# Kernel optimization log

Hardware: AMD Instinct MI355X
Metric: run time of the kernel (lower is better)

Reference implementation:

```python
import math
import jax, jax.numpy as jnp
import numpy as np

NUM_HEADS = 16
EPS = 1e-6


def _rotate_half(t):
    t1, t2 = jnp.split(t, 2, axis=-1)
    return jnp.concatenate([-t2, t1], axis=-1)


def _rmsnorm(t, w):
    # compute in fp32 like the torch module, then cast back and apply affine
    x32 = t.astype(jnp.float32)
    r = jax.lax.rsqrt(jnp.mean(x32 * x32, axis=-1, keepdims=True) + EPS)
    return (x32 * r).astype(t.dtype) * w


def setup_inputs() -> dict:
    key = jax.random.key(0)
    ks = jax.random.split(key, 12)
    B, N, C, T = 8, 1024, 1024, 1024
    hd2 = (C // NUM_HEADS) // 2  # 32
    inp = {
        "x": jax.random.normal(ks[0], (B, N, C), jnp.float32),
        "temb": jax.random.normal(ks[1], (B, T), jnp.float32),
        "cos_y": jax.random.uniform(ks[2], (1, 1, N, hd2), jnp.float32, -1.0, 1.0),
        "sin_y": jax.random.uniform(ks[3], (1, 1, N, hd2), jnp.float32, -1.0, 1.0),
        "cos_x": jax.random.uniform(ks[4], (1, 1, N, hd2), jnp.float32, -1.0, 1.0),
        "sin_x": jax.random.uniform(ks[5], (1, 1, N, hd2), jnp.float32, -1.0, 1.0),
        # params; weights stored (in, out) so y = x @ W + b (== torch x @ W.T)
        "Wqkv": jax.random.normal(ks[6], (C, 3 * C), jnp.float32) * 0.02,
        "bqkv": jnp.zeros((3 * C,), jnp.float32),
        "Wt": jax.random.normal(ks[7], (T, 3 * C), jnp.float32) * 0.02,
        "bt": jnp.zeros((3 * C,), jnp.float32),
        "Wp": jax.random.normal(ks[8], (C, C), jnp.float32) * 0.02,
        "bp": jnp.zeros((C,), jnp.float32),
        "qn_w": jnp.ones((C // NUM_HEADS,), jnp.float32),
        "kn_w": jnp.ones((C // NUM_HEADS,), jnp.float32),
    }
    return inp


def reference(x, temb, cos_y, sin_y, cos_x, sin_x,
              Wqkv, bqkv, Wt, bt, Wp, bp, qn_w, kn_w):
    B, N, C = x.shape
    H = NUM_HEADS
    hd = C // H
    # fused QKV projection + additive time conditioning
    qkv = x @ Wqkv + bqkv + (temb @ Wt + bt)[:, None, :]         # [B,N,3C]
    qkv = qkv.reshape(B, N, 3, H, hd).transpose(2, 0, 3, 1, 4)    # [3,B,H,N,hd]
    q, k, v = qkv[0], qkv[1], qkv[2]
    # per-head QK RMSNorm with affine
    q = _rmsnorm(q, qn_w)
    k = _rmsnorm(k, kn_w)
    # axial 2D RoPE on the y-half and x-half of head_dim
    qy, qx = jnp.split(q, 2, axis=-1)
    ky, kx = jnp.split(k, 2, axis=-1)
    qy = qy * cos_y + _rotate_half(qy) * sin_y
    ky = ky * cos_y + _rotate_half(ky) * sin_y
    qx = qx * cos_x + _rotate_half(qx) * sin_x
    kx = kx * cos_x + _rotate_half(kx) * sin_x
    q = jnp.concatenate([qy, qx], axis=-1)
    k = jnp.concatenate([ky, kx], axis=-1)
    # scaled dot-product attention (no dropout at eval)
    scale = 1.0 / math.sqrt(hd)
    scores = jnp.einsum('bhqd,bhkd->bhqk', q, k) * scale
    attn = jax.nn.softmax(scores, axis=-1)
    out = jnp.einsum('bhqk,bhkd->bhqd', attn, v)                  # [B,H,N,hd]
    out = out.transpose(0, 2, 1, 3).reshape(B, N, C)
    return out @ Wp + bp
```

## Files before the change

kernel.cpp:

```cpp
#include <hip/hip_runtime.h>
#include <cstdint>

typedef unsigned short u16;
typedef __bf16 bf16x8 __attribute__((ext_vector_type(8)));
typedef float f32x4 __attribute__((ext_vector_type(4)));

__device__ __forceinline__ u16 f2bf(float f) {
  __bf16 h = (__bf16)f;
  return __builtin_bit_cast(u16, h);
}
__device__ __forceinline__ float bf2f(u16 u) {
  union { uint32_t u; float f; } v; v.u = ((uint32_t)u) << 16;
  return v.f;
}

__device__ __forceinline__ void gload16(const void* g, const void* l) {
  __builtin_amdgcn_global_load_lds(
      (const __attribute__((address_space(1))) uint32_t*)(uintptr_t)g,
      (__attribute__((address_space(3))) uint32_t*)(uintptr_t)l, 16, 0, 0);
}

__device__ __forceinline__ f32x4 mfma16(bf16x8 a, bf16x8 b, f32x4 c) {
  return __builtin_amdgcn_mfma_f32_16x16x32_bf16(a, b, c, 0, 0, 0);
}

__device__ __forceinline__ int swz(int row, int col) {
  return row * 64 + ((((col >> 3) ^ (row & 7)) << 3) | (col & 7));
}

__global__ __launch_bounds__(256)
void k_cvt(const float* __restrict__ src, u16* __restrict__ dst, int n4) {
  int i = blockIdx.x * 256 + threadIdx.x;
  if (i >= n4) return;
  float4 v = ((const float4*)src)[i];
  union { u16 s[4]; uint2 u; } o;
  o.s[0] = f2bf(v.x); o.s[1] = f2bf(v.y); o.s[2] = f2bf(v.z); o.s[3] = f2bf(v.w);
  ((uint2*)dst)[i] = o.u;
}

__global__ __launch_bounds__(256)
void k_transpose(const float* __restrict__ src, u16* __restrict__ dst, int R, int Cc) {
  __shared__ u16 t[64 * 66];
  int r0 = blockIdx.y * 64, c0 = blockIdx.x * 64;
  #pragma unroll
  for (int i = 0; i < 16; i++) {
    int e = i * 256 + threadIdx.x;
    int rl = e >> 6, cl = e & 63;
    t[cl * 66 + rl] = f2bf(src[(size_t)(r0 + rl) * Cc + c0 + cl]);
  }
  __syncthreads();
  #pragma unroll
  for (int i = 0; i < 16; i++) {
    int e = i * 256 + threadIdx.x;
    int ro = e >> 6, co = e & 63;
    dst[(size_t)(c0 + ro) * R + r0 + co] = t[ro * 66 + co];
  }
}

__global__ __launch_bounds__(256)
void k_temb_part(const float* __restrict__ temb, const float* __restrict__ Wt,
                 float* __restrict__ part) {
  const int j = blockIdx.x * 256 + threadIdx.x;
  const int k0 = blockIdx.y * 32;
  float acc[8];
  #pragma unroll
  for (int b = 0; b < 8; b++) acc[b] = 0.f;
  #pragma unroll 4
  for (int k = k0; k < k0 + 32; k++) {
    float wv = Wt[(size_t)k * 3072 + j];
    #pragma unroll
    for (int b = 0; b < 8; b++) acc[b] += temb[b * 1024 + k] * wv;
  }
  float* p = part + (size_t)blockIdx.y * 24576 + j;
  #pragma unroll
  for (int b = 0; b < 8; b++) p[b * 3072] = acc[b];
}

__global__ __launch_bounds__(256)
void k_temb_red(const float* __restrict__ part, const float* __restrict__ bt,
                const float* __restrict__ bqkv, float* __restrict__ tcomb) {
  const int j = blockIdx.x * 256 + threadIdx.x;
  const int b = blockIdx.y;
  const float* p = part + b * 3072 + j;
  float a = bt[j] + bqkv[j];
  #pragma unroll
  for (int kt = 0; kt < 32; kt++) a += p[(size_t)kt * 24576];
  tcomb[b * 3072 + j] = a;
}

template <int MODE>
__global__ __launch_bounds__(512, 2)
void k_gemm(const u16* __restrict__ A, const u16* __restrict__ Bt,
            u16* __restrict__ outb, float* __restrict__ outf,
            const float* __restrict__ bias, int K, int Ntot) {
  __shared__ __align__(16) u16 As[3][128 * 64];
  __shared__ __align__(16) u16 Bs[3][256 * 64];

  const int nb = (int)gridDim.x;
  const int bid = (int)blockIdx.x;
  const int sb = (bid & 7) * (nb >> 3) + (bid >> 3);
  const int NBN = Ntot >> 8;
  const int m0 = (sb / NBN) * 128;
  const int n0 = (sb % NBN) * 256;

  const int lane = threadIdx.x & 63;
  const int w = threadIdx.x >> 6;
  const int wm = w >> 2;
  const int wn = w & 3;
  const int l15 = lane & 15;
  const int g8 = (lane >> 4) * 8;
  const int lr = lane >> 3;
  const int schunk = ((lane & 7) ^ lr) * 8;

  const u16* Ag = A + (size_t)(m0 + w * 16 + lr) * K + schunk;
  const u16* Bg = Bt + (size_t)(n0 + lr) * K + schunk;

  f32x4 acc[4][4];
  #pragma unroll
  for (int i = 0; i < 4; i++)
    #pragma unroll
    for (int j = 0; j < 4; j++) acc[i][j] = (f32x4){0.f, 0.f, 0.f, 0.f};

  auto stageA_Blo = [&](int kt_, int buf_) {
    const int ko = kt_ << 6;
    #pragma unroll
    for (int t = 0; t < 2; t++) {
      int r0 = w * 16 + t * 8;
      gload16(Ag + (size_t)(t * 8) * K + ko, &As[buf_][r0 * 64]);
    }
    #pragma unroll
    for (int t = 0; t < 2; t++) {
      int f0 = w * 16 + t * 8;
      int r0 = (f0 >> 5) * 64 + (f0 & 31);
      gload16(Bg + (size_t)r0 * K + ko, &Bs[buf_][r0 * 64]);
    }
  };
  auto stageBhi = [&](int kt_, int buf_) {
    const int ko = kt_ << 6;
    #pragma unroll
    for (int t = 0; t < 2; t++) {
      int f0 = w * 16 + t * 8;
      int r0 = (f0 >> 5) * 64 + 32 + (f0 & 31);
      gload16(Bg + (size_t)r0 * K + ko, &Bs[buf_][r0 * 64]);
    }
  };

  const int NT = K >> 6;
  stageA_Blo(0, 0); stageBhi(0, 0);
  stageA_Blo(1, 1); stageBhi(1, 1);
  asm volatile("s_waitcnt vmcnt(8)" ::: "memory");
  __builtin_amdgcn_s_barrier();
  asm volatile("" ::: "memory");

  int cur = 0;
  for (int kt = 0; kt < NT; kt++) {
    const int nxtbuf = cur + 2 >= 3 ? cur - 1 : cur + 2;

    bf16x8 af[2][4], bfr[2][4];
    #pragma unroll
    for (int s = 0; s < 2; s++)
      #pragma unroll
      for (int mf = 0; mf < 4; mf++)
        af[s][mf] = *(const bf16x8*)&As[cur][swz(wm * 64 + mf * 16 + l15, s * 32 + g8)];
    #pragma unroll
    for (int s = 0; s < 2; s++)
      #pragma unroll
      for (int nf = 0; nf < 2; nf++)
        bfr[s][nf] = *(const bf16x8*)&Bs[cur][swz(wn * 64 + nf * 16 + l15, s * 32 + g8)];
    if (kt + 2 < NT) stageA_Blo(kt + 2, nxtbuf);
    if (kt <= NT - 2) asm volatile("s_waitcnt vmcnt(6)" ::: "memory");
    else              asm volatile("s_waitcnt vmcnt(0)" ::: "memory");
    __builtin_amdgcn_s_barrier();
    asm volatile("" ::: "memory");
    __builtin_amdgcn_s_setprio(1);
    #pragma unroll
    for (int s = 0; s < 2; s++)
      #pragma unroll
      for (int mf = 0; mf < 4; mf++)
        #pragma unroll
        for (int nf = 0; nf < 2; nf++)
          acc[mf][nf] = mfma16(af[s][mf], bfr[s][nf], acc[mf][nf]);
    __builtin_amdgcn_s_setprio(0);

    #pragma unroll
    for (int s = 0; s < 2; s++)
      #pragma unroll
      for (int nf = 2; nf < 4; nf++)
        bfr[s][nf] = *(const bf16x8*)&Bs[cur][swz(wn * 64 + nf * 16 + l15, s * 32 + g8)];
    if (kt + 2 < NT) stageBhi(kt + 2, nxtbuf);
    if (kt < NT - 2)       asm volatile("s_waitcnt vmcnt(6)" ::: "memory");
    else if (kt == NT - 2) asm volatile("s_waitcnt vmcnt(2)" ::: "memory");
    else                   asm volatile("s_waitcnt vmcnt(0)" ::: "memory");
    __builtin_amdgcn_s_barrier();
    asm volatile("" ::: "memory");
    __builtin_amdgcn_s_setprio(1);
    #pragma unroll
    for (int s = 0; s < 2; s++)
      #pragma unroll
      for (int mf = 0; mf < 4; mf++)
        #pragma unroll
        for (int nf = 2; nf < 4; nf++)
          acc[mf][nf] = mfma16(af[s][mf], bfr[s][nf], acc[mf][nf]);
    __builtin_amdgcn_s_setprio(0);

    cur = cur + 1 >= 3 ? 0 : cur + 1;
  }

  const int rl = (lane >> 4) * 4;
  #pragma unroll
  for (int mf = 0; mf < 4; mf++) {
    #pragma unroll
    for (int nf = 0; nf < 4; nf++) {
      #pragma unroll
      for (int r = 0; r < 4; r++) {
        int grow = m0 + wm * 64 + mf * 16 + rl + r;
        int gcol = n0 + wn * 64 + nf * 16 + l15;
        float v = acc[mf][nf][r];
        if (MODE == 0) {
          int b = grow >> 10;
          v += bias[b * Ntot + gcol];
          outb[(size_t)grow * Ntot + gcol] = f2bf(v);
        } else {
          v += bias[gcol];
          outf[(size_t)grow * Ntot + gcol] = v;
        }
      }
    }
  }
}

__global__ __launch_bounds__(256)
void k_rrv(const u16* __restrict__ qkv,
           const float* __restrict__ cos_y, const float* __restrict__ sin_y,
           const float* __restrict__ cos_x, const float* __restrict__ sin_x,
           const float* __restrict__ qn_w, const float* __restrict__ kn_w,
           u16* __restrict__ Qo, u16* __restrict__ Ko, u16* __restrict__ VT) {
  __shared__ u16 t[64 * 68];
  const int n0 = blockIdx.x * 64, h = blockIdx.y, b = blockIdx.z;
  const int bh = b * 16 + h;
  const int lane = threadIdx.x & 63, w = threadIdx.x >> 6;
  const int l15 = lane & 15, lg = lane >> 4;
  float4 qw = *(const float4*)(qn_w + l15 * 4);
  float4 kw = *(const float4*)(kn_w + l15 * 4);
  const float sgn = (lane & 4) ? 1.0f : -1.0f;
  const float* ct = (lane & 8) ? cos_x : cos_y;
  const float* st = (lane & 8) ? sin_x : sin_y;
  const float QSCALE = 0.18033688011112042f;

  #pragma unroll
  for (int rr = 0; rr < 4; rr++) {
    int row = n0 + w * 16 + rr * 4 + lg;
    size_t src = (size_t)(b * 1024 + row) * 3072 + h * 64 + l15 * 4;
    uint2 qu = *(const uint2*)(qkv + src);
    uint2 ku = *(const uint2*)(qkv + src + 1024);
    float q[4], k[4];
    q[0] = bf2f((u16)qu.x); q[1] = bf2f((u16)(qu.x >> 16));
    q[2] = bf2f((u16)qu.y); q[3] = bf2f((u16)(qu.y >> 16));
    k[0] = bf2f((u16)ku.x); k[1] = bf2f((u16)(ku.x >> 16));
    k[2] = bf2f((u16)ku.y); k[3] = bf2f((u16)(ku.y >> 16));
    float sq = q[0]*q[0] + q[1]*q[1] + q[2]*q[2] + q[3]*q[3];
    float sk = k[0]*k[0] + k[1]*k[1] + k[2]*k[2] + k[3]*k[3];
    #pragma unroll
    for (int m = 1; m < 16; m <<= 1) {
      sq += __shfl_xor(sq, m);
      sk += __shfl_xor(sk, m);
    }
    float rq = rsqrtf(sq * (1.0f / 64.0f) + 1e-6f);
    float rk = rsqrtf(sk * (1.0f / 64.0f) + 1e-6f);
    float4 cc = *(const float4*)(ct + (size_t)row * 32 + (lane & 7) * 4);
    float4 ss = *(const float4*)(st + (size_t)row * 32 + (lane & 7) * 4);
    float qn[4], kn[4];
    qn[0] = q[0]*rq*qw.x; qn[1] = q[1]*rq*qw.y; qn[2] = q[2]*rq*qw.z; qn[3] = q[3]*rq*qw.w;
    kn[0] = k[0]*rk*kw.x; kn[1] = k[1]*rk*kw.y; kn[2] = k[2]*rk*kw.z; kn[3] = k[3]*rk*kw.w;
    float c[4] = {cc.x, cc.y, cc.z, cc.w};
    float s[4] = {ss.x, ss.y, ss.z, ss.w};
    union { u16 e[4]; uint2 u; } oq, ok;
    #pragma unroll
    for (int j = 0; j < 4; j++) {
      float qp = __shfl_xor(qn[j], 4);
      float kp = __shfl_xor(kn[j], 4);
      oq.e[j] = f2bf((qn[j] * c[j] + sgn * qp * s[j]) * QSCALE);
      ok.e[j] = f2bf(kn[j] * c[j] + sgn * kp * s[j]);
    }
    size_t dst = ((size_t)bh * 1024 + row) * 64 + l15 * 4;
    *(uint2*)(Qo + dst) = oq.u;
    *(uint2*)(Ko + dst) = ok.u;
  }

  #pragma unroll
  for (int i = 0; i < 4; i++) {
    int e = i * 256 + threadIdx.x;
    int n = e >> 4, dc = e & 15;
    uint2 v = *(const uint2*)(qkv + (size_t)(b * 1024 + n0 + n) * 3072 + 2048 + h * 64 + dc * 4);
    t[(dc * 4 + 0) * 68 + n] = (u16)v.x;
    t[(dc * 4 + 1) * 68 + n] = (u16)(v.x >> 16);
    t[(dc * 4 + 2) * 68 + n] = (u16)v.y;
    t[(dc * 4 + 3) * 68 + n] = (u16)(v.y >> 16);
  }
  __syncthreads();
  #pragma unroll
  for (int i = 0; i < 4; i++) {
    int e = i * 256 + threadIdx.x;
    int d = e >> 4, nc = e & 15;
    const u16* p = &t[d * 68 + nc * 4];
    uint2 o;
    o.x = (uint32_t)p[0] | ((uint32_t)p[1] << 16);
    o.y = (uint32_t)p[2] | ((uint32_t)p[3] << 16);
    *(uint2*)(VT + ((size_t)bh * 64 + d) * 1024 + n0 + nc * 4) = o;
  }
}

__global__ __launch_bounds__(256, 2)
void k_attn(const u16* __restrict__ Q, const u16* __restrict__ Kb,
            const u16* __restrict__ VT, u16* __restrict__ Ob) {
  __shared__ u16 Ks[2][4096], VTs[2][4096], Ps[4][2048];
  const int lane = threadIdx.x & 63;
  const int w = threadIdx.x >> 6;
  const int bh = blockIdx.x;
  const int qt = blockIdx.y;
  const int b = bh >> 4, h = bh & 15;
  const size_t base = (size_t)bh * 65536;
  const int q0 = qt * 128;
  const int scol = ((lane & 7) ^ (lane >> 3)) * 8;
  const int lr = lane >> 3;

  bf16x8 aq[2][2];
  #pragma unroll
  for (int i = 0; i < 2; i++)
    #pragma unroll
    for (int s = 0; s < 2; s++)
      aq[i][s] = *(const bf16x8*)(Q + base +
          (size_t)(q0 + w * 32 + i * 16 + (lane & 15)) * 64 + s * 32 + (lane >> 4) * 8);

  f32x4 acc_o[2][4];
  float lpar[2][4];
  #pragma unroll
  for (int i = 0; i < 2; i++)
    #pragma unroll
    for (int r = 0; r < 4; r++) {
      acc_o[i][r] = (f32x4){0.f, 0.f, 0.f, 0.f};
      lpar[i][r] = 0.f;
    }

  #pragma unroll
  for (int tt = 0; tt < 2; tt++) {
    int t = w * 2 + tt;
    gload16(Kb + base + (size_t)(8 * t + lr) * 64 + scol, &Ks[0][t * 512]);
    gload16(VT + base + (size_t)(8 * t + lr) * 1024 + scol, &VTs[0][t * 512]);
  }

  for (int it = 0; it < 16; it++) {
    __syncthreads();
    const int cur = it & 1;
    if (it < 15) {
      const int nxt = cur ^ 1;
      const int j1 = (it + 1) * 64;
      #pragma unroll
      for (int tt = 0; tt < 2; tt++) {
        int t = w * 2 + tt;
        gload16(Kb + base + (size_t)(j1 + 8 * t + lr) * 64 + scol, &Ks[nxt][t * 512]);
        gload16(VT + base + (size_t)(8 * t + lr) * 1024 + j1 + scol, &VTs[nxt][t * 512]);
      }
    }
    const u16* K_ = Ks[cur];
    const u16* V_ = VTs[cur];

    f32x4 accs[2][4];
    #pragma unroll
    for (int i = 0; i < 2; i++)
      #pragma unroll
      for (int nt = 0; nt < 4; nt++) accs[i][nt] = (f32x4){0.f, 0.f, 0.f, 0.f};
    #pragma unroll
    for (int s = 0; s < 2; s++) {
      bf16x8 bk[4];
      #pragma unroll
      for (int nt = 0; nt < 4; nt++)
        bk[nt] = *(const bf16x8*)&K_[swz(nt * 16 + (lane & 15), s * 32 + (lane >> 4) * 8)];
      #pragma unroll
      for (int i = 0; i < 2; i++)
        #pragma unroll
        for (int nt = 0; nt < 4; nt++)
          accs[i][nt] = mfma16(aq[i][s], bk[nt], accs[i][nt]);
    }

    #pragma unroll
    for (int i = 0; i < 2; i++) {
      #pragma unroll
      for (int nt = 0; nt < 4; nt++) {
        #pragma unroll
        for (int r = 0; r < 4; r++) {
          float p = __builtin_amdgcn_exp2f(accs[i][nt][r]);
          lpar[i][r] += p;
          Ps[w][swz(i * 16 + (lane >> 4) * 4 + r, nt * 16 + (lane & 15))] = f2bf(p);
        }
      }
    }
    asm volatile("s_waitcnt lgkmcnt(0)" ::: "memory");

    #pragma unroll
    for (int s = 0; s < 2; s++) {
      bf16x8 bv[4];
      #pragma unroll
      for (int dt = 0; dt < 4; dt++)
        bv[dt] = *(const bf16x8*)&V_[swz(dt * 16 + (lane & 15), s * 32 + (lane >> 4) * 8)];
      #pragma unroll
      for (int i = 0; i < 2; i++) {
        bf16x8 ap = *(const bf16x8*)&Ps[w][swz(i * 16 + (lane & 15), s * 32 + (lane >> 4) * 8)];
        #pragma unroll
        for (int dt = 0; dt < 4; dt++)
          acc_o[i][dt] = mfma16(ap, bv[dt], acc_o[i][dt]);
      }
    }
  }

  #pragma unroll
  for (int i = 0; i < 2; i++) {
    float inv[4];
    #pragma unroll
    for (int r = 0; r < 4; r++) {
      float l = lpar[i][r];
      #pragma unroll
      for (int m = 1; m < 16; m <<= 1) l += __shfl_xor(l, m);
      inv[r] = 1.0f / l;
    }
    #pragma unroll
    for (int dt = 0; dt < 4; dt++)
      #pragma unroll
      for (int r = 0; r < 4; r++) {
        int row = q0 + w * 32 + i * 16 + (lane >> 4) * 4 + r;
        int col = h * 64 + dt * 16 + (lane & 15);
        Ob[((size_t)b * 1024 + row) * 1024 + col] = f2bf(acc_o[i][dt][r] * inv[r]);
      }
  }
}

extern "C" void kernel_launch(void* const* d_in, const int* in_sizes, int n_in,
                              void* d_out, int out_size, void* d_ws, size_t ws_size,
                              hipStream_t stream) {
  const float* x     = (const float*)d_in[0];
  const float* temb  = (const float*)d_in[1];
  const float* cos_y = (const float*)d_in[2];
  const float* sin_y = (const float*)d_in[3];
  const float* cos_x = (const float*)d_in[4];
  const float* sin_x = (const float*)d_in[5];
  const float* Wqkv  = (const float*)d_in[6];
  const float* bqkv  = (const float*)d_in[7];
  const float* Wt    = (const float*)d_in[8];
  const float* bt    = (const float*)d_in[9];
  const float* Wp    = (const float*)d_in[10];
  const float* bp    = (const float*)d_in[11];
  const float* qn_w  = (const float*)d_in[12];
  const float* kn_w  = (const float*)d_in[13];
  float* out = (float*)d_out;

  char* ws = (char*)d_ws;
  u16*   x_bf  = (u16*)(ws);
  u16*   WqkvT = (u16*)(ws + 16777216);
  u16*   WpT   = (u16*)(ws + 23068672);
  float* tcomb = (float*)(ws + 25165824);
  u16*   qkv   = (u16*)(ws + 25264128);
  u16*   Qb    = (u16*)(ws + 75595776);
  u16*   Kb    = (u16*)(ws + 92372992);
  u16*   VTb   = (u16*)(ws + 109150208);
  float* tpart = (float*)(ws + 125927424);
  u16*   att   = x_bf;

  k_cvt<<<8192, 256, 0, stream>>>(x, x_bf, 8192 * 1024 / 4);
  k_transpose<<<dim3(48, 16), 256, 0, stream>>>(Wqkv, WqkvT, 1024, 3072);
  k_transpose<<<dim3(16, 16), 256, 0, stream>>>(Wp, WpT, 1024, 1024);
  k_temb_part<<<dim3(12, 32), 256, 0, stream>>>(temb, Wt, tpart);
  k_temb_red<<<dim3(12, 8), 256, 0, stream>>>(tpart, bt, bqkv, tcomb);
  k_gemm<0><<<dim3(768), 512, 0, stream>>>(x_bf, WqkvT, qkv, nullptr, tcomb, 1024, 3072);
  k_rrv<<<dim3(16, 16, 8), 256, 0, stream>>>(qkv, cos_y, sin_y, cos_x, sin_x,
                                             qn_w, kn_w, Qb, Kb, VTb);
  k_attn<<<dim3(128, 8), 256, 0, stream>>>(Qb, Kb, VTb, att);
  k_gemm<1><<<dim3(256), 512, 0, stream>>>(att, WpT, nullptr, out, bp, 1024, 1024);
}
```

Baseline: 284.0 us.

## Merge prep kernels into one launch, fold temb reduction into GEMM, prioritize attention MFMAs

```diff
diff --git a/kernel.cpp b/kernel.cpp
--- a/kernel.cpp
+++ b/kernel.cpp
@@ -28,20 +28,9 @@
   return row * 64 + ((((col >> 3) ^ (row & 7)) << 3) | (col & 7));
 }
 
-__global__ __launch_bounds__(256)
-void k_cvt(const float* __restrict__ src, u16* __restrict__ dst, int n4) {
-  int i = blockIdx.x * 256 + threadIdx.x;
-  if (i >= n4) return;
-  float4 v = ((const float4*)src)[i];
-  union { u16 s[4]; uint2 u; } o;
-  o.s[0] = f2bf(v.x); o.s[1] = f2bf(v.y); o.s[2] = f2bf(v.z); o.s[3] = f2bf(v.w);
-  ((uint2*)dst)[i] = o.u;
-}
-
-__global__ __launch_bounds__(256)
-void k_transpose(const float* __restrict__ src, u16* __restrict__ dst, int R, int Cc) {
-  __shared__ u16 t[64 * 66];
-  int r0 = blockIdx.y * 64, c0 = blockIdx.x * 64;
+__device__ __forceinline__ void transpose64(const float* __restrict__ src,
+                                            u16* __restrict__ dst, int R, int Cc,
+                                            int r0, int c0, u16* t) {
   #pragma unroll
   for (int i = 0; i < 16; i++) {
     int e = i * 256 + threadIdx.x;
@@ -58,43 +47,60 @@
 }
 
 __global__ __launch_bounds__(256)
-void k_temb_part(const float* __restrict__ temb, const float* __restrict__ Wt,
-                 float* __restrict__ part) {
-  const int j = blockIdx.x * 256 + threadIdx.x;
-  const int k0 = blockIdx.y * 32;
-  float acc[8];
-  #pragma unroll
-  for (int b = 0; b < 8; b++) acc[b] = 0.f;
-  #pragma unroll 4
-  for (int k = k0; k < k0 + 32; k++) {
-    float wv = Wt[(size_t)k * 3072 + j];
-    #pragma unroll
-    for (int b = 0; b < 8; b++) acc[b] += temb[b * 1024 + k] * wv;
-  }
-  float* p = part + (size_t)blockIdx.y * 24576 + j;
-  #pragma unroll
-  for (int b = 0; b < 8; b++) p[b * 3072] = acc[b];
-}
-
-__global__ __launch_bounds__(256)
-void k_temb_red(const float* __restrict__ part, const float* __restrict__ bt,
-                const float* __restrict__ bqkv, float* __restrict__ tcomb) {
-  const int j = blockIdx.x * 256 + threadIdx.x;
-  const int b = blockIdx.y;
-  const float* p = part + b * 3072 + j;
-  float a = bt[j] + bqkv[j];
-  #pragma unroll
-  for (int kt = 0; kt < 32; kt++) a += p[(size_t)kt * 24576];
-  tcomb[b * 3072 + j] = a;
+void k_prep(const float* __restrict__ x, u16* __restrict__ x_bf,
+            const float* __restrict__ Wqkv, u16* __restrict__ WqkvT,
+            const float* __restrict__ Wp, u16* __restrict__ WpT,
+            const float* __restrict__ temb, const float* __restrict__ Wt,
+            float* __restrict__ tpart) {
+  __shared__ u16 t[64 * 66];
+  int bid = blockIdx.x;
+  if (bid < 8192) {
+    int i = bid * 256 + threadIdx.x;
+    float4 v = ((const float4*)x)[i];
+    union { u16 s[4]; uint2 u; } o;
+    o.s[0] = f2bf(v.x); o.s[1] = f2bf(v.y); o.s[2] = f2bf(v.z); o.s[3] = f2bf(v.w);
+    ((uint2*)x_bf)[i] = o.u;
+    return;
+  }
+  bid -= 8192;
+  if (bid < 768) {
+    transpose64(Wqkv, WqkvT, 1024, 3072, (bid / 48) * 64, (bid % 48) * 64, t);
+    return;
+  }
+  bid -= 768;
+  if (bid < 256) {
+    transpose64(Wp, WpT, 1024, 1024, (bid / 16) * 64, (bid % 16) * 64, t);
+    return;
+  }
+  bid -= 256;
+  {
+    const int j = (bid % 12) * 256 + threadIdx.x;
+    const int k0 = (bid / 12) * 32;
+    float acc[8];
+    #pragma unroll
+    for (int b = 0; b < 8; b++) acc[b] = 0.f;
+    #pragma unroll 4
+    for (int k = k0; k < k0 + 32; k++) {
+      float wv = Wt[(size_t)k * 3072 + j];
+      #pragma unroll
+      for (int b = 0; b < 8; b++) acc[b] += temb[b * 1024 + k] * wv;
+    }
+    float* p = tpart + (size_t)(bid / 12) * 24576 + j;
+    #pragma unroll
+    for (int b = 0; b < 8; b++) p[b * 3072] = acc[b];
+  }
 }
 
 template <int MODE>
 __global__ __launch_bounds__(512, 2)
 void k_gemm(const u16* __restrict__ A, const u16* __restrict__ Bt,
             u16* __restrict__ outb, float* __restrict__ outf,
-            const float* __restrict__ bias, int K, int Ntot) {
+            const float* __restrict__ bias,
+            const float* __restrict__ bt, const float* __restrict__ bqkv,
+            const float* __restrict__ tpart, int K, int Ntot) {
   __shared__ __align__(16) u16 As[3][128 * 64];
   __shared__ __align__(16) u16 Bs[3][256 * 64];
+  __shared__ float tcs[256];
 
   const int nb = (int)gridDim.x;
   const int bid = (int)blockIdx.x;
@@ -114,6 +120,18 @@
 
   const u16* Ag = A + (size_t)(m0 + w * 16 + lr) * K + schunk;
   const u16* Bg = Bt + (size_t)(n0 + lr) * K + schunk;
+
+  if (MODE == 0) {
+    if (threadIdx.x < 256) {
+      const int bidx = m0 >> 10;
+      const int j = n0 + (int)threadIdx.x;
+      float a = bt[j] + bqkv[j];
+      #pragma unroll
+      for (int kt = 0; kt < 32; kt++) a += tpart[(size_t)kt * 24576 + bidx * 3072 + j];
+      tcs[threadIdx.x] = a;
+    }
+    asm volatile("" ::: "memory");
+  }
 
   f32x4 acc[4][4];
   #pragma unroll
@@ -217,8 +235,7 @@
         int gcol = n0 + wn * 64 + nf * 16 + l15;
         float v = acc[mf][nf][r];
         if (MODE == 0) {
-          int b = grow >> 10;
-          v += bias[b * Ntot + gcol];
+          v += tcs[wn * 64 + nf * 16 + l15];
           outb[(size_t)grow * Ntot + gcol] = f2bf(v);
         } else {
           v += bias[gcol];
@@ -376,11 +393,13 @@
       #pragma unroll
       for (int nt = 0; nt < 4; nt++)
         bk[nt] = *(const bf16x8*)&K_[swz(nt * 16 + (lane & 15), s * 32 + (lane >> 4) * 8)];
+      __builtin_amdgcn_s_setprio(1);
       #pragma unroll
       for (int i = 0; i < 2; i++)
         #pragma unroll
         for (int nt = 0; nt < 4; nt++)
           accs[i][nt] = mfma16(aq[i][s], bk[nt], accs[i][nt]);
+      __builtin_amdgcn_s_setprio(0);
     }
 
     #pragma unroll
@@ -403,13 +422,15 @@
       #pragma unroll
       for (int dt = 0; dt < 4; dt++)
         bv[dt] = *(const bf16x8*)&V_[swz(dt * 16 + (lane & 15), s * 32 + (lane >> 4) * 8)];
-      #pragma unroll
-      for (int i = 0; i < 2; i++) {
-        bf16x8 ap = *(const bf16x8*)&Ps[w][swz(i * 16 + (lane & 15), s * 32 + (lane >> 4) * 8)];
-        #pragma unroll
-        for (int dt = 0; dt < 4; dt++)
-          acc_o[i][dt] = mfma16(ap, bv[dt], acc_o[i][dt]);
+      bf16x8 ap0 = *(const bf16x8*)&Ps[w][swz(0 * 16 + (lane & 15), s * 32 + (lane >> 4) * 8)];
+      bf16x8 ap1 = *(const bf16x8*)&Ps[w][swz(1 * 16 + (lane & 15), s * 32 + (lane >> 4) * 8)];
+      __builtin_amdgcn_s_setprio(1);
+      #pragma unroll
+      for (int dt = 0; dt < 4; dt++) {
+        acc_o[0][dt] = mfma16(ap0, bv[dt], acc_o[0][dt]);
+        acc_o[1][dt] = mfma16(ap1, bv[dt], acc_o[1][dt]);
       }
+      __builtin_amdgcn_s_setprio(0);
     }
   }
 
@@ -457,7 +478,6 @@
   u16*   x_bf  = (u16*)(ws);
   u16*   WqkvT = (u16*)(ws + 16777216);
   u16*   WpT   = (u16*)(ws + 23068672);
-  float* tcomb = (float*)(ws + 25165824);
   u16*   qkv   = (u16*)(ws + 25264128);
   u16*   Qb    = (u16*)(ws + 75595776);
   u16*   Kb    = (u16*)(ws + 92372992);
@@ -465,14 +485,12 @@
   float* tpart = (float*)(ws + 125927424);
   u16*   att   = x_bf;
 
-  k_cvt<<<8192, 256, 0, stream>>>(x, x_bf, 8192 * 1024 / 4);
-  k_transpose<<<dim3(48, 16), 256, 0, stream>>>(Wqkv, WqkvT, 1024, 3072);
-  k_transpose<<<dim3(16, 16), 256, 0, stream>>>(Wp, WpT, 1024, 1024);
-  k_temb_part<<<dim3(12, 32), 256, 0, stream>>>(temb, Wt, tpart);
-  k_temb_red<<<dim3(12, 8), 256, 0, stream>>>(tpart, bt, bqkv, tcomb);
-  k_gemm<0><<<dim3(768), 512, 0, stream>>>(x_bf, WqkvT, qkv, nullptr, tcomb, 1024, 3072);
+  k_prep<<<9600, 256, 0, stream>>>(x, x_bf, Wqkv, WqkvT, Wp, WpT, temb, Wt, tpart);
+  k_gemm<0><<<dim3(768), 512, 0, stream>>>(x_bf, WqkvT, qkv, nullptr, nullptr,
+                                           bt, bqkv, tpart, 1024, 3072);
   k_rrv<<<dim3(16, 16, 8), 256, 0, stream>>>(qkv, cos_y, sin_y, cos_x, sin_x,
                                              qn_w, kn_w, Qb, Kb, VTb);
   k_attn<<<dim3(128, 8), 256, 0, stream>>>(Qb, Kb, VTb, att);
-  k_gemm<1><<<dim3(256), 512, 0, stream>>>(att, WpT, nullptr, out, bp, 1024, 1024);
-}
+  k_gemm<1><<<dim3(256), 512, 0, stream>>>(att, WpT, nullptr, out, bp,
+                                           nullptr, nullptr, nullptr, 1024, 1024);
+}
```

Result: faster. 273.2 us (-3.8%).
